# Performance work log

Measured on AMD Instinct MI355X. Metric: run time of the kernel, lower is better.

## Reference

```python
import jax, jax.numpy as jnp
import numpy as np

EMBED = 64
HEADS = 2
HDIM = EMBED // HEADS  # 32
IN_FEAT = 256
NODES = 3


def _lin(x, W, b=None):
    y = x @ W.T
    return y + b if b is not None else y


def setup_inputs() -> dict:
    key = jax.random.key(0)
    ks = jax.random.split(key, 24)
    B = 131072
    s = 0.05
    inp = {
        "spatial": jax.random.normal(ks[0], (B, IN_FEAT), jnp.float32),
        "genomic": jax.random.normal(ks[1], (B, IN_FEAT), jnp.float32),
        "temporal": jax.random.normal(ks[2], (B, IN_FEAT), jnp.float32),
        "adj_matrix": jnp.ones((B, NODES, NODES), jnp.float32),
        # modality projections (Linear(256,64))
        "Wsp": jax.random.normal(ks[3], (EMBED, IN_FEAT)) * s,
        "bsp": jnp.zeros((EMBED,)),
        "Wge": jax.random.normal(ks[4], (EMBED, IN_FEAT)) * s,
        "bge": jnp.zeros((EMBED,)),
        "Wtm": jax.random.normal(ks[5], (EMBED, IN_FEAT)) * s,
        "btm": jnp.zeros((EMBED,)),
        # GAT: W Linear(64,64,no bias), attention Linear(2*head_dim=64 -> 1, no bias)
        "gat_W": jax.random.normal(ks[6], (EMBED, EMBED)) * s,
        "gat_a": jax.random.normal(ks[7], (2 * HDIM,)) * s,
        # MultiheadAttention(64, 2)
        "in_w": jax.random.normal(ks[8], (3 * EMBED, EMBED)) * s,
        "in_b": jnp.zeros((3 * EMBED,)),
        "out_w": jax.random.normal(ks[9], (EMBED, EMBED)) * s,
        "out_b": jnp.zeros((EMBED,)),
        # LayerNorm(64)
        "ln_g": jnp.ones((EMBED,)),
        "ln_b": jnp.zeros((EMBED,)),
        # predictor 64->32->16->2
        "p1_w": jax.random.normal(ks[10], (32, EMBED)) * s,
        "p1_b": jnp.zeros((32,)),
        "p2_w": jax.random.normal(ks[11], (16, 32)) * s,
        "p2_b": jnp.zeros((16,)),
        "p3_w": jax.random.normal(ks[12], (2, 16)) * s,
        "p3_b": jnp.zeros((2,)),
    }
    return inp


def reference(spatial, genomic, temporal, adj_matrix,
              Wsp, bsp, Wge, bge, Wtm, btm,
              gat_W, gat_a, in_w, in_b, out_w, out_b,
              ln_g, ln_b, p1_w, p1_b, p2_w, p2_b, p3_w, p3_b):
    # Dropout layers are identity in eval mode.
    B = spatial.shape[0]
    sp = jax.nn.relu(_lin(spatial, Wsp, bsp))   # [B, 64]
    ge = jax.nn.relu(_lin(genomic, Wge, bge))
    tm = jax.nn.relu(_lin(temporal, Wtm, btm))
    x = jnp.stack([sp, ge, tm], axis=1)          # [B, 3, 64]

    # ---- GAT layer (dense attention over 3 nodes, 2 heads) ----
    h = _lin(x, gat_W).reshape(B, NODES, HEADS, HDIM)  # [B,3,H,D]
    # a . concat(h_i, h_j) decomposes into a1.h_i + a2.h_j
    e_i = jnp.einsum('bnhd,d->bnh', h, gat_a[:HDIM])
    e_j = jnp.einsum('bnhd,d->bnh', h, gat_a[HDIM:])
    e = e_i[:, :, None, :] + e_j[:, None, :, :]        # [B,3,3,H]
    e = jnp.where(e > 0, e, 0.2 * e)                    # LeakyReLU(0.2)
    e = jnp.where(adj_matrix[..., None] == 0, -1e9, e)
    alpha = jax.nn.softmax(e, axis=2)                   # softmax over j
    h_out = jnp.einsum('bijh,bjhd->bihd', alpha, h).reshape(B, NODES, EMBED)
    gat_pooled = h_out.mean(axis=1)                     # [B, 64]

    # ---- Cross-modal MHA + residual LayerNorm ----
    qkv = _lin(x, in_w, in_b)                           # [B,3,192]
    q, k, v = jnp.split(qkv, 3, axis=-1)
    def heads(t):
        return t.reshape(B, NODES, HEADS, HDIM).transpose(0, 2, 1, 3)
    q, k, v = heads(q), heads(k), heads(v)              # [B,H,3,D]
    sc = jnp.einsum('bhqd,bhkd->bhqk', q, k) / jnp.sqrt(jnp.float32(HDIM))
    attn = jax.nn.softmax(sc, axis=-1)
    o = jnp.einsum('bhqk,bhkd->bhqd', attn, v).transpose(0, 2, 1, 3).reshape(B, NODES, EMBED)
    attn_out = _lin(o, out_w, out_b)
    y = x + attn_out
    mu = y.mean(-1, keepdims=True)
    var = ((y - mu) ** 2).mean(-1, keepdims=True)
    y = (y - mu) / jnp.sqrt(var + 1e-5) * ln_g + ln_b
    cross_modal = y.mean(axis=1)                        # [B, 64]

    # ---- Predictor ----
    combined = gat_pooled + cross_modal
    z = jax.nn.relu(_lin(combined, p1_w, p1_b))
    z = jax.nn.relu(_lin(z, p2_w, p2_b))
    out = _lin(z, p3_w, p3_b)                           # [B, 2]
    return out[:, 0], out[:, 1]
```

## Files before the change

kernel.cpp:

```cpp
#include <hip/hip_runtime.h>

typedef __attribute__((ext_vector_type(8))) short v8s;
typedef __attribute__((ext_vector_type(4))) float v4f;

#define MFMA16(a, b, c) __builtin_amdgcn_mfma_f32_16x16x32_bf16((a), (b), (c), 0, 0, 0)
#define SCQ 0.17677669529663687f

__device__ __forceinline__ short f2bf(float f) {
    unsigned u = __float_as_uint(f);
    u += 0x7FFFu + ((u >> 16) & 1u);
    return (short)(u >> 16);
}
__device__ __forceinline__ float bf2f(short s) {
    return __uint_as_float(((unsigned)(unsigned short)s) << 16);
}
__device__ __forceinline__ float bfly16(float v) {
#pragma unroll
    for (int m = 1; m < 16; m <<= 1) v += __shfl_xor(v, m);
    return v;
}

__global__ void giman_prep(const float* __restrict__ Wsp, const float* __restrict__ Wge,
                           const float* __restrict__ Wtm, const float* __restrict__ gatW,
                           const float* __restrict__ gat_a,
                           const float* __restrict__ inw, const float* __restrict__ outw,
                           const float* __restrict__ p1w, const float* __restrict__ p2w,
                           const float* __restrict__ in_b, const float* __restrict__ out_b,
                           short* __restrict__ ws) {
    int idx = blockIdx.x * 256 + threadIdx.x;
    if (idx < 73216) {
        int j = idx & 7, l = (idx >> 3) & 63;
        int lr = l & 15, lc = ((l >> 4) << 3) + j;
        float val;
        if (idx < 49152) {
            const float* W; int off;
            if (idx < 16384)      { W = Wsp; off = idx; }
            else if (idx < 32768) { W = Wge; off = idx - 16384; }
            else                  { W = Wtm; off = idx - 32768; }
            int t = off >> 9, kk = t & 7, nb = t >> 3;
            val = W[(nb * 16 + lr) * 256 + kk * 32 + lc];
        } else if (idx < 54272) {
            int t = (idx - 49152) >> 9, kk = t & 1, nb = t >> 1;
            if (nb < 4) {
                val = gatW[(nb * 16 + lr) * 64 + kk * 32 + lc];
            } else {
                int f = kk * 32 + lc;
                val = 0.f;
                if (lr < 4) {
                    float s = 0.f;
                    for (int d = 0; d < 32; ++d)
                        s += gat_a[(lr >> 1) * 32 + d] * gatW[((lr & 1) * 32 + d) * 64 + f];
                    val = s;
                } else if (lr < 6) {
                    int h = lr - 4;
                    float s = 0.f;
                    for (int d = 0; d < 32; ++d)
                        s += inw[(32 * h + d) * 64 + f] * in_b[64 + 32 * h + d];
                    val = s * SCQ;
                } else if (lr < 8) {
                    int h = lr - 6;
                    float s = 0.f;
                    for (int d = 0; d < 32; ++d)
                        s += inw[(64 + 32 * h + d) * 64 + f] * in_b[32 * h + d];
                    val = s * SCQ;
                }
            }
        } else if (idx < 62464) {
            int t = (idx - 54272) >> 9, kk = t & 1, nbh = t >> 1;
            int h = nbh >> 2, nb = nbh & 3;
            int a = kk * 32 + lc, b = nb * 16 + lr;
            float s = 0.f;
            for (int d = 0; d < 32; ++d)
                s += inw[(32 * h + d) * 64 + a] * inw[(64 + 32 * h + d) * 64 + b];
            val = s * SCQ;
        } else if (idx < 70656) {
            int t = (idx - 62464) >> 9, kk = t & 1, nbh = t >> 1;
            int h = nbh >> 2, nb = nbh & 3;
            int r = nb * 16 + lr, c = kk * 32 + lc;
            float s = 0.f;
            for (int k = 0; k < 32; ++k)
                s += outw[r * 64 + h * 32 + k] * inw[(128 + h * 32 + k) * 64 + c];
            val = s;
        } else if (idx < 72704) {
            int t = (idx - 70656) >> 9, kk = t & 1, nb = t >> 1;
            val = p1w[(nb * 16 + lr) * 64 + kk * 32 + lc];
        } else {
            val = p2w[lr * 32 + lc];
        }
        ws[idx] = f2bf(val);
    } else if (idx < 73280) {
        int r = idx - 73216;
        float s = out_b[r];
        for (int k = 0; k < 64; ++k) s += outw[r * 64 + 128 + k] * in_b[128 + k];
        ((float*)(ws + 73216))[r] = s;
    } else if (idx < 73282) {
        int h = idx - 73280;
        float s = 0.f;
        for (int d = 0; d < 32; ++d) s += in_b[32 * h + d] * in_b[64 + 32 * h + d];
        ((float*)(ws + 73216))[64 + h] = s * SCQ;
    }
}

__global__ __launch_bounds__(256)
void giman_proj(const float* __restrict__ spatial, const float* __restrict__ genomic,
                const float* __restrict__ temporal,
                const float* __restrict__ bsp, const float* __restrict__ bge,
                const float* __restrict__ btm,
                const short* __restrict__ wf, short* __restrict__ xg, int Btot)
{
    const int wv = threadIdx.x >> 6;
    const int lane = threadIdx.x & 63;
    const int lq = lane & 15, lg = lane >> 4;
    const int nG = Btot >> 6;
    const int nItems = 3 * nG;

    for (int it = blockIdx.x; it < nItems; it += gridDim.x) {
        const int m = it / nG;
        const int g = it - m * nG;
        const int s0 = g * 64 + wv * 16;

        const float* X = (m == 0 ? spatial : (m == 1 ? genomic : temporal))
                       + (size_t)(s0 + lq) * 256 + lg * 8;
        const float* Bm = (m == 0 ? bsp : (m == 1 ? bge : btm));
        const v8s* bwf = (const v8s*)(wf + m * 16384);

        float4 L[16];
#pragma unroll
        for (int k = 0; k < 8; ++k) {
            L[2 * k]     = *(const float4*)(X + k * 32);
            L[2 * k + 1] = *(const float4*)(X + k * 32 + 4);
        }

        v4f acc[4];
#pragma unroll
        for (int nb = 0; nb < 4; ++nb) acc[nb] = (v4f){0.f, 0.f, 0.f, 0.f};

#pragma unroll
        for (int kk = 0; kk < 8; ++kk) {
            v8s af;
            af[0] = f2bf(L[2 * kk].x); af[1] = f2bf(L[2 * kk].y);
            af[2] = f2bf(L[2 * kk].z); af[3] = f2bf(L[2 * kk].w);
            af[4] = f2bf(L[2 * kk + 1].x); af[5] = f2bf(L[2 * kk + 1].y);
            af[6] = f2bf(L[2 * kk + 1].z); af[7] = f2bf(L[2 * kk + 1].w);
#pragma unroll
            for (int nb = 0; nb < 4; ++nb)
                acc[nb] = MFMA16(af, bwf[(nb * 8 + kk) * 64 + lane], acc[nb]);
        }

        float bb0 = Bm[lq], bb1 = Bm[16 + lq], bb2 = Bm[32 + lq], bb3 = Bm[48 + lq];
#pragma unroll
        for (int nb = 0; nb < 4; ++nb) {
            float bb = nb == 0 ? bb0 : (nb == 1 ? bb1 : (nb == 2 ? bb2 : bb3));
#pragma unroll
            for (int r = 0; r < 4; ++r) {
                float v = acc[nb][r] + bb;
                v = v > 0.f ? v : 0.f;
                xg[((size_t)(s0 + 4 * lg + r) * 3 + m) * 64 + nb * 16 + lq] = f2bf(v);
            }
        }
    }
}

__global__ __launch_bounds__(256)
void giman_main(const float* __restrict__ adj, const short* __restrict__ wf,
                const short* __restrict__ xg,
                const float* __restrict__ ln_g, const float* __restrict__ ln_b,
                const float* __restrict__ p1b, const float* __restrict__ p2b,
                const float* __restrict__ p3w, const float* __restrict__ p3bb,
                float* __restrict__ dout, int Btot)
{
    __shared__ __align__(16) short x_lds[4][48][72];
    __shared__ __align__(16) short v_lds[4][16][72];
    __shared__ __align__(16) float a_lds[4][148];

    const int wv   = threadIdx.x >> 6;
    const int lane = threadIdx.x & 63;
    const int lq   = lane & 15;
    const int lg   = lane >> 4;
    const int grpb = lane & 48;
    const int s0   = blockIdx.x * 64 + wv * 16;
    if (s0 + 16 > Btot) return;

    short (*xw)[72] = x_lds[wv];
    short (*vtr)[72] = v_lds[wv];

    if (lane < 36)
        *(float4*)&a_lds[wv][lane * 4] = *(const float4*)(adj + (size_t)s0 * 9 + lane * 4);

    {
        const short* xsrc = xg + (size_t)s0 * 192;
#pragma unroll
        for (int i = 0; i < 6; ++i) {
            int c = lane + 64 * i;
            v8s val = *(const v8s*)(xsrc + c * 8);
            *(v8s*)&xw[c >> 3][(c & 7) * 8] = val;
        }
    }

    const float* cbp = (const float*)(wf + 73216);
    float cbv[4], lgv[4], lbv[4];
#pragma unroll
    for (int nb = 0; nb < 4; ++nb) {
        int c = nb * 16 + lq;
        cbv[nb] = cbp[c];
        lgv[nb] = ln_g[c];
        lbv[nb] = ln_b[c];
    }
    const float gmv0 = cbp[64], gmv1 = cbp[65];
    const float inv3 = 1.f / 3.f;

    const v8s* gwf = (const v8s*)(wf + 49152);
    const v8s* pff = (const v8s*)(wf + 54272);
    const v8s* uf  = (const v8s*)(wf + 62464);

#pragma unroll 1
    for (int t = 0; t < 4; ++t) {
        int rn = lq & 3; rn = (rn == 3) ? 2 : rn;
        const short* xrp = xw[(t * 4 + (lq >> 2)) * 3 + rn];
        v8s xa0 = *(const v8s*)(xrp + lg * 8);
        v8s xa1 = *(const v8s*)(xrp + 32 + lg * 8);

        float gp[4];
        v4f eacc = (v4f){0.f, 0.f, 0.f, 0.f};
        {
            v4f hacc[4];
#pragma unroll
            for (int nb = 0; nb < 4; ++nb) {
                v4f a = (v4f){0.f, 0.f, 0.f, 0.f};
                a = MFMA16(xa0, gwf[(nb * 2 + 0) * 64 + lane], a);
                a = MFMA16(xa1, gwf[(nb * 2 + 1) * 64 + lane], a);
                hacc[nb] = a;
            }
            eacc = MFMA16(xa0, gwf[8 * 64 + lane], eacc);
            eacc = MFMA16(xa1, gwf[9 * 64 + lane], eacc);

            const float* amp = &a_lds[wv][(t * 4 + lg) * 9];
            float wj0[2], wj1[2], wj2[2];
#pragma unroll
            for (int h = 0; h < 2; ++h) {
                float ei0 = __shfl(eacc[0], grpb + h);
                float ei1 = __shfl(eacc[1], grpb + h);
                float ei2 = __shfl(eacc[2], grpb + h);
                float ej0 = __shfl(eacc[0], grpb + 2 + h);
                float ej1 = __shfl(eacc[1], grpb + 2 + h);
                float ej2 = __shfl(eacc[2], grpb + 2 + h);
                float w0 = 0.f, w1 = 0.f, w2 = 0.f;
#pragma unroll
                for (int i = 0; i < 3; ++i) {
                    float eiv = i == 0 ? ei0 : (i == 1 ? ei1 : ei2);
                    float e0 = eiv + ej0; e0 = e0 > 0.f ? e0 : 0.2f * e0; if (amp[i * 3 + 0] == 0.f) e0 = -1e9f;
                    float e1 = eiv + ej1; e1 = e1 > 0.f ? e1 : 0.2f * e1; if (amp[i * 3 + 1] == 0.f) e1 = -1e9f;
                    float e2 = eiv + ej2; e2 = e2 > 0.f ? e2 : 0.2f * e2; if (amp[i * 3 + 2] == 0.f) e2 = -1e9f;
                    float mx = fmaxf(e0, fmaxf(e1, e2));
                    float q0 = __expf(e0 - mx), q1 = __expf(e1 - mx), q2 = __expf(e2 - mx);
                    float inv = 1.f / (q0 + q1 + q2);
                    w0 += q0 * inv; w1 += q1 * inv; w2 += q2 * inv;
                }
                wj0[h] = w0; wj1[h] = w1; wj2[h] = w2;
            }
#pragma unroll
            for (int nb = 0; nb < 4; ++nb) {
                int h = nb >> 1;
                gp[nb] = (wj0[h] * hacc[nb][0] + wj1[h] * hacc[nb][1] + wj2[h] * hacc[nb][2]) * inv3;
            }
        }

        float y[4][3];
#pragma unroll
        for (int nb = 0; nb < 4; ++nb)
#pragma unroll
            for (int r = 0; r < 3; ++r)
                y[nb][r] = bf2f(xw[(t * 4 + lg) * 3 + r][nb * 16 + lq]) + cbv[nb];

        const int sb = grpb + (grpb >> 2);
#pragma unroll
        for (int h = 0; h < 2; ++h) {
            {
                v4f va[4];
#pragma unroll
                for (int nb = 0; nb < 4; ++nb) {
                    v4f a = (v4f){0.f, 0.f, 0.f, 0.f};
                    a = MFMA16(xa0, pff[((h * 4 + nb) * 2 + 0) * 64 + lane], a);
                    a = MFMA16(xa1, pff[((h * 4 + nb) * 2 + 1) * 64 + lane], a);
                    va[nb] = a;
                }
#pragma unroll
                for (int nb = 0; nb < 4; ++nb)
#pragma unroll
                    for (int r = 0; r < 3; ++r)
                        vtr[lg * 4 + r][nb * 16 + lq] = f2bf(va[nb][r]);
            }
            v8s aq0 = *(const v8s*)&vtr[lq][lg * 8];
            v8s aq1 = *(const v8s*)&vtr[lq][32 + lg * 8];
            v4f S = (v4f){0.f, 0.f, 0.f, 0.f};
            S = MFMA16(aq0, xa0, S);
            S = MFMA16(aq1, xa1, S);

            float alh[9];
            {
                float gm = h ? gmv1 : gmv0;
                float bv0 = __shfl(eacc[0], grpb + 6 + h) + gm;
                float bv1 = __shfl(eacc[1], grpb + 6 + h) + gm;
                float bv2 = __shfl(eacc[2], grpb + 6 + h) + gm;
#pragma unroll
                for (int i = 0; i < 3; ++i) {
                    float av = __shfl(eacc[i], grpb + 4 + h);
                    float e0 = __shfl(S[i], sb + 0) + av + bv0;
                    float e1 = __shfl(S[i], sb + 1) + av + bv1;
                    float e2 = __shfl(S[i], sb + 2) + av + bv2;
                    float mx = fmaxf(e0, fmaxf(e1, e2));
                    float w0 = __expf(e0 - mx), w1 = __expf(e1 - mx), w2 = __expf(e2 - mx);
                    float inv = 1.f / (w0 + w1 + w2);
                    alh[i * 3 + 0] = w0 * inv;
                    alh[i * 3 + 1] = w1 * inv;
                    alh[i * 3 + 2] = w2 * inv;
                }
            }

#pragma unroll
            for (int nb = 0; nb < 4; ++nb) {
                v4f u = (v4f){0.f, 0.f, 0.f, 0.f};
                u = MFMA16(xa0, uf[((h * 4 + nb) * 2 + 0) * 64 + lane], u);
                u = MFMA16(xa1, uf[((h * 4 + nb) * 2 + 1) * 64 + lane], u);
#pragma unroll
                for (int r = 0; r < 3; ++r)
                    y[nb][r] += alh[r * 3 + 0] * u[0] + alh[r * 3 + 1] * u[1]
                              + alh[r * 3 + 2] * u[2];
            }
        }

        float mu[3], rs[3];
#pragma unroll
        for (int r = 0; r < 3; ++r) {
            float sm = y[0][r] + y[1][r] + y[2][r] + y[3][r];
            float sq = y[0][r] * y[0][r] + y[1][r] * y[1][r]
                     + y[2][r] * y[2][r] + y[3][r] * y[3][r];
            sm = bfly16(sm); sq = bfly16(sq);
            float m_ = sm * (1.f / 64.f);
            float var = sq * (1.f / 64.f) - m_ * m_;
            mu[r] = m_;
            rs[r] = rsqrtf(var + 1e-5f);
        }
#pragma unroll
        for (int nb = 0; nb < 4; ++nb) {
            float cm = (y[nb][0] - mu[0]) * rs[0] + (y[nb][1] - mu[1]) * rs[1]
                     + (y[nb][2] - mu[2]) * rs[2];
            float comb = gp[nb] + cm * inv3 * lgv[nb] + lbv[nb];
            xw[t * 4 + lg][nb * 16 + lq] = f2bf(comb);
        }
    }

    {
        const v8s* p1f = (const v8s*)(wf + 70656);
        const v8s* p2f = (const v8s*)(wf + 72704);
        short (*zw)[40] = (short (*)[40])(&xw[16][0]);
        const short* crp = &xw[lq][0];
        v8s ca0 = *(const v8s*)(crp + lg * 8);
        v8s ca1 = *(const v8s*)(crp + 32 + lg * 8);
        const float pb1v0 = p1b[lq], pb1v1 = p1b[16 + lq], pb2v = p2b[lq];
        const float p3w0 = p3w[lq], p3w1 = p3w[16 + lq];
        v4f z1[2];
#pragma unroll
        for (int nb = 0; nb < 2; ++nb) {
            float bb = nb ? pb1v1 : pb1v0;
            v4f a = (v4f){bb, bb, bb, bb};
            a = MFMA16(ca0, p1f[(nb * 2 + 0) * 64 + lane], a);
            a = MFMA16(ca1, p1f[(nb * 2 + 1) * 64 + lane], a);
            z1[nb] = a;
        }
#pragma unroll
        for (int nb = 0; nb < 2; ++nb)
#pragma unroll
            for (int r = 0; r < 4; ++r) {
                float v = z1[nb][r];
                v = v > 0.f ? v : 0.f;
                zw[lg * 4 + r][nb * 16 + lq] = f2bf(v);
            }
        v8s za = *(const v8s*)(&zw[lq][0] + lg * 8);
        v4f z2 = (v4f){pb2v, pb2v, pb2v, pb2v};
        z2 = MFMA16(za, p2f[lane], z2);
        const float p3b0 = p3bb[0], p3b1 = p3bb[1];
#pragma unroll
        for (int r = 0; r < 4; ++r) {
            float v = z2[r];
            v = v > 0.f ? v : 0.f;
            float po0 = bfly16(v * p3w0);
            float po1 = bfly16(v * p3w1);
            if (lq == 0) {
                dout[s0 + lg * 4 + r] = po0 + p3b0;
                dout[Btot + s0 + lg * 4 + r] = po1 + p3b1;
            }
        }
    }
}

extern "C" void kernel_launch(void* const* d_in, const int* in_sizes, int n_in,
                              void* d_out, int out_size, void* d_ws, size_t ws_size,
                              hipStream_t stream) {
    const float* spatial  = (const float*)d_in[0];
    const float* genomic  = (const float*)d_in[1];
    const float* temporal = (const float*)d_in[2];
    const float* adj      = (const float*)d_in[3];
    const float* Wsp = (const float*)d_in[4];
    const float* bsp = (const float*)d_in[5];
    const float* Wge = (const float*)d_in[6];
    const float* bge = (const float*)d_in[7];
    const float* Wtm = (const float*)d_in[8];
    const float* btm = (const float*)d_in[9];
    const float* gatW  = (const float*)d_in[10];
    const float* gat_a = (const float*)d_in[11];
    const float* in_w  = (const float*)d_in[12];
    const float* in_b  = (const float*)d_in[13];
    const float* out_w = (const float*)d_in[14];
    const float* out_b = (const float*)d_in[15];
    const float* ln_g  = (const float*)d_in[16];
    const float* ln_b  = (const float*)d_in[17];
    const float* p1w = (const float*)d_in[18];
    const float* p1b = (const float*)d_in[19];
    const float* p2w = (const float*)d_in[20];
    const float* p2b = (const float*)d_in[21];
    const float* p3w = (const float*)d_in[22];
    const float* p3b = (const float*)d_in[23];
    float* out = (float*)d_out;
    const int Btot = in_sizes[0] / 256;

    short* wf = (short*)d_ws;
    short* xg = wf + 81920;

    giman_prep<<<(73282 + 255) / 256, 256, 0, stream>>>(Wsp, Wge, Wtm, gatW, gat_a,
                                                        in_w, out_w, p1w, p2w,
                                                        in_b, out_b, wf);
    giman_proj<<<2048, 256, 0, stream>>>(spatial, genomic, temporal,
                                         bsp, bge, btm, wf, xg, Btot);
    giman_main<<<Btot / 64, 256, 0, stream>>>(adj, wf, xg,
                                              ln_g, ln_b, p1b, p2b, p3w, p3b,
                                              out, Btot);
}
```

Baseline: 233.1 us.

## Stage projection inputs through LDS via direct global-to-LDS loads

The projection kernel now copies 32-row input tiles straight into shared memory with global_load_lds, replacing the per-lane strided float4 register loads. Work is split so that each wave pair handles 16 rows and each wave computes 32 of the 64 output columns. The grid is halved and two block barriers per tile are added. The aim is fully coalesced row loads and lower register pressure, at the cost of LDS traffic, synchronisation and no overlap between the load and compute of successive tiles.

```diff
diff --git a/kernel.cpp b/kernel.cpp
--- a/kernel.cpp
+++ b/kernel.cpp
@@ -18,6 +18,10 @@
 #pragma unroll
     for (int m = 1; m < 16; m <<= 1) v += __shfl_xor(v, m);
     return v;
+}
+__device__ __forceinline__ void gload16(const float* g, float* l) {
+    __builtin_amdgcn_global_load_lds((const __attribute__((address_space(1))) void*)g,
+                                     (__attribute__((address_space(3))) void*)l, 16, 0, 0);
 }
 
 __global__ void giman_prep(const float* __restrict__ Wsp, const float* __restrict__ Wge,
@@ -108,56 +112,58 @@
                 const float* __restrict__ btm,
                 const short* __restrict__ wf, short* __restrict__ xg, int Btot)
 {
+    __shared__ __align__(16) float xs[32][260];
+
     const int wv = threadIdx.x >> 6;
     const int lane = threadIdx.x & 63;
     const int lq = lane & 15, lg = lane >> 4;
-    const int nG = Btot >> 6;
+    const int half = wv & 1;
+    const int nbp  = wv >> 1;
+    const int nG = Btot >> 5;
     const int nItems = 3 * nG;
 
     for (int it = blockIdx.x; it < nItems; it += gridDim.x) {
         const int m = it / nG;
         const int g = it - m * nG;
-        const int s0 = g * 64 + wv * 16;
-
-        const float* X = (m == 0 ? spatial : (m == 1 ? genomic : temporal))
-                       + (size_t)(s0 + lq) * 256 + lg * 8;
+        const int s0 = g * 32;
+
+        const float* Xm = (m == 0 ? spatial : (m == 1 ? genomic : temporal));
+        const float* src = Xm + (size_t)s0 * 256;
         const float* Bm = (m == 0 ? bsp : (m == 1 ? bge : btm));
         const v8s* bwf = (const v8s*)(wf + m * 16384);
 
-        float4 L[16];
-#pragma unroll
-        for (int k = 0; k < 8; ++k) {
-            L[2 * k]     = *(const float4*)(X + k * 32);
-            L[2 * k + 1] = *(const float4*)(X + k * 32 + 4);
-        }
-
-        v4f acc[4];
-#pragma unroll
-        for (int nb = 0; nb < 4; ++nb) acc[nb] = (v4f){0.f, 0.f, 0.f, 0.f};
-
+#pragma unroll
+        for (int i = 0; i < 8; ++i) {
+            int row = wv * 8 + i;
+            gload16(src + row * 256 + lane * 4, &xs[row][0]);
+        }
+        __syncthreads();
+
+        v4f acc0 = (v4f){0.f, 0.f, 0.f, 0.f};
+        v4f acc1 = (v4f){0.f, 0.f, 0.f, 0.f};
 #pragma unroll
         for (int kk = 0; kk < 8; ++kk) {
+            const float* rp = &xs[half * 16 + lq][kk * 32 + lg * 8];
+            float4 u = *(const float4*)rp;
+            float4 v = *(const float4*)(rp + 4);
             v8s af;
-            af[0] = f2bf(L[2 * kk].x); af[1] = f2bf(L[2 * kk].y);
-            af[2] = f2bf(L[2 * kk].z); af[3] = f2bf(L[2 * kk].w);
-            af[4] = f2bf(L[2 * kk + 1].x); af[5] = f2bf(L[2 * kk + 1].y);
-            af[6] = f2bf(L[2 * kk + 1].z); af[7] = f2bf(L[2 * kk + 1].w);
-#pragma unroll
-            for (int nb = 0; nb < 4; ++nb)
-                acc[nb] = MFMA16(af, bwf[(nb * 8 + kk) * 64 + lane], acc[nb]);
-        }
-
-        float bb0 = Bm[lq], bb1 = Bm[16 + lq], bb2 = Bm[32 + lq], bb3 = Bm[48 + lq];
-#pragma unroll
-        for (int nb = 0; nb < 4; ++nb) {
-            float bb = nb == 0 ? bb0 : (nb == 1 ? bb1 : (nb == 2 ? bb2 : bb3));
-#pragma unroll
-            for (int r = 0; r < 4; ++r) {
-                float v = acc[nb][r] + bb;
-                v = v > 0.f ? v : 0.f;
-                xg[((size_t)(s0 + 4 * lg + r) * 3 + m) * 64 + nb * 16 + lq] = f2bf(v);
-            }
-        }
+            af[0] = f2bf(u.x); af[1] = f2bf(u.y); af[2] = f2bf(u.z); af[3] = f2bf(u.w);
+            af[4] = f2bf(v.x); af[5] = f2bf(v.y); af[6] = f2bf(v.z); af[7] = f2bf(v.w);
+            acc0 = MFMA16(af, bwf[((nbp * 2 + 0) * 8 + kk) * 64 + lane], acc0);
+            acc1 = MFMA16(af, bwf[((nbp * 2 + 1) * 8 + kk) * 64 + lane], acc1);
+        }
+
+        float bb0 = Bm[nbp * 32 + lq], bb1 = Bm[nbp * 32 + 16 + lq];
+#pragma unroll
+        for (int r = 0; r < 4; ++r) {
+            int row = s0 + half * 16 + 4 * lg + r;
+            size_t base = ((size_t)row * 3 + m) * 64 + nbp * 32 + lq;
+            float v0 = acc0[r] + bb0; v0 = v0 > 0.f ? v0 : 0.f;
+            float v1 = acc1[r] + bb1; v1 = v1 > 0.f ? v1 : 0.f;
+            xg[base] = f2bf(v0);
+            xg[base + 16] = f2bf(v1);
+        }
+        __syncthreads();
     }
 }
 
@@ -430,7 +436,7 @@
     giman_prep<<<(73282 + 255) / 256, 256, 0, stream>>>(Wsp, Wge, Wtm, gatW, gat_a,
                                                         in_w, out_w, p1w, p2w,
                                                         in_b, out_b, wf);
-    giman_proj<<<2048, 256, 0, stream>>>(spatial, genomic, temporal,
+    giman_proj<<<1024, 256, 0, stream>>>(spatial, genomic, temporal,
                                          bsp, bge, btm, wf, xg, Btot);
     giman_main<<<Btot / 64, 256, 0, stream>>>(adj, wf, xg,
                                               ln_g, ln_b, p1b, p2b, p3w, p3b,
```

Result: faster. 221.3 us (-5.1%).
